# Kernel optimization log

Measured on AMD Instinct MI355X. Metric: run time of the kernel, lower is better.

The kernel has to match this reference:

```python
import jax, jax.numpy as jnp
import numpy as np

B, S, E, H = 2, 2048, 1024, 16
HD = E // H  # head dim = 64
BASE = 10000.0


def _rope(x):
    # x: [b, h, s, hd]; interleaved RoPE (pairs (2i, 2i+1) rotated)
    s, hd = x.shape[-2], x.shape[-1]
    theta = 1.0 / (BASE ** (jnp.arange(0, hd, 2, dtype=jnp.float32) / hd))  # [hd/2]
    enc = jnp.arange(s, dtype=jnp.float32)[:, None] * theta[None, :]        # [s, hd/2]
    enc = jnp.repeat(enc, 2, axis=-1)                                        # [s, hd] interleaved
    cos, sin = jnp.cos(enc), jnp.sin(enc)
    # rotate_half: (x1, x2) -> (-x2, x1) on interleaved pairs
    xp = x.reshape(*x.shape[:-1], hd // 2, 2)
    rot = jnp.stack((-xp[..., 1], xp[..., 0]), axis=-1).reshape(x.shape)
    return x * cos + rot * sin


def reference(x, w1, w2):
    b, s, e = x.shape
    qkv = jnp.einsum('bse,fe->bsf', x, w1)                 # [b, s, 3e]
    qkv = qkv.reshape(b, s, 3, H, HD)                      # 'b s (n h e)'
    q, k, v = (jnp.transpose(qkv[:, :, i], (0, 2, 1, 3)) for i in range(3))  # [b,h,s,hd]
    q, k = _rope(q), _rope(k)
    scale = 1.0 / jnp.sqrt(jnp.asarray(HD, dtype=x.dtype))
    scores = jnp.einsum('bhqd,bhkd->bhqk', q, k) * scale   # [b,h,s,s]
    attn = jax.nn.softmax(scores, axis=-1)
    o = jnp.einsum('bhqk,bhkd->bhqd', attn, v)             # [b,h,s,hd]
    o = jnp.transpose(o, (0, 2, 1, 3)).reshape(b, s, e)    # 'b h s e -> b s (h e)'
    return jnp.einsum('bse,fe->bsf', o, w2)


def setup_inputs() -> dict:
    key = jax.random.key(0)
    k1, k2, k3 = jax.random.split(key, 3)
    x = jax.random.normal(k1, (B, S, E), dtype=jnp.float32)
    w1 = jax.random.normal(k2, (3 * E, E), dtype=jnp.float32) * (E ** -0.5)
    w2 = jax.random.normal(k3, (E, E), dtype=jnp.float32) * (E ** -0.5)
    return {"x": x, "w1": w1, "w2": w2}
```

## Files before the change

kernel.cpp:

```cpp
#include <hip/hip_runtime.h>
#include <math.h>

typedef unsigned short u16;
typedef unsigned int u32;
typedef float f32x4 __attribute__((ext_vector_type(4)));
typedef float f32x16 __attribute__((ext_vector_type(16)));
typedef u32 u32x4 __attribute__((ext_vector_type(4)));

static const size_t TAB_B  = 0;
static const size_t QBF_B  = 524288;
static const size_t KBF_B  = 8912896;
static const size_t VTB_B  = 17301504;
static const size_t W2H_B  = 25690112;
static const size_t XBF_B  = 29884416;
static const size_t W1BF_B = 38273024;
static const size_t O16_B  = 29884416;

#if __has_builtin(__builtin_amdgcn_exp2f)
#define EXP2(x) __builtin_amdgcn_exp2f(x)
#else
#define EXP2(x) __expf(0.69314718056f * (x))
#endif

__device__ __forceinline__ u16 f2bf(float f) {
  u32 u = __builtin_bit_cast(u32, f);
  u += 0x7fffu + ((u >> 16) & 1u);
  return (u16)(u >> 16);
}
__device__ __forceinline__ float bf2f(u16 h) {
  return __builtin_bit_cast(float, (u32)h << 16);
}
__device__ __forceinline__ u16 f2h(float f) {
  _Float16 h = (_Float16)f;
  return __builtin_bit_cast(u16, h);
}
__device__ __forceinline__ u32 cvtpk(float a, float b) {
  u32 r;
  asm("v_cvt_pk_bf16_f32 %0, %1, %2" : "=v"(r) : "v"(a), "v"(b));
  return r;
}
__device__ __forceinline__ void plswap(u32& a, u32& b) {
  asm volatile("v_permlane32_swap_b32 %0, %1" : "+v"(a), "+v"(b));
}
__device__ __forceinline__ void mfma16(f32x4& d, u32x4 a, u32x4 b) {
  asm volatile("v_mfma_f32_16x16x32_bf16 %0, %1, %2, %0"
               : "+v"(d)
               : "v"(a), "v"(b));
}
__device__ __forceinline__ void mfma16f(f32x4& d, u32x4 a, u32x4 b) {
  asm volatile("v_mfma_f32_16x16x32_f16 %0, %1, %2, %0"
               : "+v"(d)
               : "v"(a), "v"(b));
}
__device__ __forceinline__ void mfma32(f32x16& d, u32x4 a, u32x4 b) {
  asm volatile("v_mfma_f32_32x32x16_bf16 %0, %1, %2, %0"
               : "+v"(d)
               : "v"(a), "v"(b));
}
__device__ __forceinline__ void gld16(const void* g, void* l) {
  __builtin_amdgcn_global_load_lds(
      (const __attribute__((address_space(1))) void*)(void*)g,
      (__attribute__((address_space(3))) void*)l, 16, 0, 0);
}
#define HZ()                                            \
  do {                                                  \
    asm volatile("s_nop 7\ns_nop 7\ns_nop 7\ns_nop 7"); \
    __builtin_amdgcn_sched_barrier(0);                  \
  } while (0)

__global__ __launch_bounds__(256) void prep_kernel(
    const float* __restrict__ x, const float* __restrict__ w1,
    const float* __restrict__ w2, float2* __restrict__ tab,
    u16* __restrict__ xbf, u16* __restrict__ w1bf, u16* __restrict__ w2h) {
  const int blk = blockIdx.x;
  const int t = threadIdx.x;
  if (blk < 256) {
    const int idx = (blk << 8) + t;
    const int s = idx >> 5, i = idx & 31;
    double theta = pow(10000.0, -((double)(2 * i)) / 64.0);
    float ang = (float)s * (float)theta;
    tab[idx] = make_float2(cosf(ang), sinf(ang));
  } else if (blk < 1280) {
    int i = ((blk - 256) << 8) + t;
#pragma unroll
    for (int r = 0; r < 4; ++r, i += 262144) {
      float4 v = ((const float4*)x)[i];
      ushort4 o;
      o.x = f2bf(v.x); o.y = f2bf(v.y); o.z = f2bf(v.z); o.w = f2bf(v.w);
      ((ushort4*)xbf)[i] = o;
    }
  } else if (blk < 2048) {
    int i = ((blk - 1280) << 8) + t;
#pragma unroll
    for (int r = 0; r < 4; ++r, i += 196608) {
      float4 v = ((const float4*)w1)[i];
      ushort4 o;
      o.x = f2bf(v.x); o.y = f2bf(v.y); o.z = f2bf(v.z); o.w = f2bf(v.w);
      ((ushort4*)w1bf)[i] = o;
    }
  } else {
    int i = ((blk - 2048) << 8) + t;
#pragma unroll
    for (int r = 0; r < 4; ++r, i += 65536) {
      float4 v = ((const float4*)w2)[i];
      ushort4 o;
      o.x = f2h(v.x); o.y = f2h(v.y); o.z = f2h(v.z); o.w = f2h(v.w);
      ((ushort4*)w2h)[i] = o;
    }
  }
}

template <int MODE>
__global__ __launch_bounds__(256) void gemm_bt(
    const u16* __restrict__ Ahi, const u16* __restrict__ Bhi, int nbn, int nkb,
    int cpx, const float2* __restrict__ tab, u16* __restrict__ qd,
    u16* __restrict__ kd, u16* __restrict__ vtd, float* __restrict__ fout) {
  __shared__ __align__(16) char SMEM[34816];
  char* As = SMEM;
  char* Bs = SMEM + 16384;
  const int bid = blockIdx.x;
  const int wgid = (bid & 7) * cpx + (bid >> 3);
  const int bm = wgid / nbn;
  const int bn = wgid % nbn;
  const int m0 = bm << 7;
  const int n0 = bn << 7;
  const int t = threadIdx.x;
  const int w = t >> 6;
  const int lane = t & 63;
  const int lr = lane & 15;
  const int lg = lane >> 4;
  const int wr0 = (w >> 1) << 6;
  const int wc0 = (w & 1) << 6;
  const int srow0 = t >> 3;
  const int sblk = t & 7;

  f32x4 acc[4][4];
#pragma unroll
  for (int mi = 0; mi < 4; ++mi)
#pragma unroll
    for (int ni = 0; ni < 4; ++ni) acc[mi][ni] = (f32x4)0.0f;

  for (int kb = 0; kb < nkb; ++kb) {
    const int k0 = kb << 6;
    if (kb) __syncthreads();
#pragma unroll
    for (int r = 0; r < 4; ++r) {
      const int row = srow0 + (r << 5);
      const int g = sblk ^ (row & 7);
      gld16(Ahi + (size_t)(m0 + row) * 1024 + k0 + (g << 3),
            As + (r << 12) + (w << 10));
      gld16(Bhi + (size_t)(n0 + row) * 1024 + k0 + (g << 3),
            Bs + (r << 12) + (w << 10));
    }
    asm volatile("s_waitcnt vmcnt(0)" ::: "memory");
    __syncthreads();
#pragma unroll
    for (int kk = 0; kk < 2; ++kk) {
      u32x4 af[4], bf[4];
#pragma unroll
      for (int mi = 0; mi < 4; ++mi) {
        const int row = wr0 + (mi << 4) + lr;
        af[mi] = *(const u32x4*)(As + row * 128 +
                                 ((((kk << 2) + lg) ^ (row & 7)) << 4));
      }
#pragma unroll
      for (int ni = 0; ni < 4; ++ni) {
        const int row = wc0 + (ni << 4) + lr;
        bf[ni] = *(const u32x4*)(Bs + row * 128 +
                                 ((((kk << 2) + lg) ^ (row & 7)) << 4));
      }
      asm volatile("s_nop 1");
      __builtin_amdgcn_s_setprio(1);
#pragma unroll
      for (int mi = 0; mi < 4; ++mi)
#pragma unroll
        for (int ni = 0; ni < 4; ++ni) {
          if constexpr (MODE == 1)
            mfma16f(acc[mi][ni], af[mi], bf[ni]);
          else
            mfma16(acc[mi][ni], af[mi], bf[ni]);
        }
      __builtin_amdgcn_s_setprio(0);
    }
  }
  HZ();
  if (MODE == 0 && n0 >= 2048) {
    u16* Vt = (u16*)SMEM;
    __syncthreads();
#pragma unroll
    for (int mi = 0; mi < 4; ++mi)
#pragma unroll
      for (int ni = 0; ni < 4; ++ni)
#pragma unroll
        for (int i = 0; i < 4; ++i) {
          const int dl = wc0 + (ni << 4) + lr;
          const int sl = wr0 + (mi << 4) + (lg << 2) + i;
          Vt[dl * 136 + sl] = f2bf(acc[mi][ni][i]);
        }
    __syncthreads();
    const int row = t >> 1;
    const int half = t & 1;
    const int hh2 = (n0 - 2048 + row) >> 6;
    const int d2 = (n0 - 2048 + row) & 63;
    const int b2 = m0 >> 11;
    u16* dst = vtd + (((size_t)(b2 * 16 + hh2) * 64 + d2) * 2048) +
               (m0 & 2047) + half * 64;
    const u16* src = Vt + row * 136 + half * 64;
#pragma unroll
    for (int c = 0; c < 8; ++c)
      *(u32x4*)(dst + (c << 3)) = *(const u32x4*)(src + (c << 3));
    return;
  }
#pragma unroll
  for (int mi = 0; mi < 4; ++mi)
#pragma unroll
    for (int ni = 0; ni < 4; ++ni)
#pragma unroll
      for (int i = 0; i < 4; ++i) {
        float val = acc[mi][ni][i];
        const int grow = m0 + wr0 + (mi << 4) + (lg << 2) + i;
        const int col = n0 + wc0 + (ni << 4) + lr;
        if (MODE == 0) {
          const int b = grow >> 11, s = grow & 2047;
          const int which = col >> 10, hh = (col >> 6) & 15, d = col & 63;
          const size_t base = (size_t)((b << 4) + hh);
          float other = __shfl_xor(val, 1);
          float2 cs = tab[(s << 5) + (d >> 1)];
          float r = (d & 1) ? fmaf(val, cs.x, other * cs.y)
                            : fmaf(val, cs.x, -other * cs.y);
          if (which == 0) r *= 0.18033688011f;
          u16* dstp = which ? kd : qd;
          dstp[(base * 2048 + s) * 64 + d] = f2bf(r);
        } else {
          fout[(size_t)grow * 1024 + col] = val;
        }
      }
}

__global__ __launch_bounds__(256) void attn_mfma(
    const u16* __restrict__ q, const u16* __restrict__ k,
    const u16* __restrict__ vt, u16* __restrict__ o16) {
  __shared__ __align__(16) char Ks[2][8192];
  __shared__ __align__(16) char Vs[2][8192];
  const int bid = blockIdx.x;
  const int swz = (bid & 7) * 64 + (bid >> 3);
  const int qt = swz & 15;
  const int hh = (swz >> 4) & 15;
  const int b = swz >> 8;
  const int t = threadIdx.x;
  const int w = t >> 6;
  const int lane = t & 63;
  const int lq = lane & 31;
  const int h = lane >> 5;

  const size_t bh = (size_t)((b << 4) + hh);
  const u16* qb = q + (bh * 2048 + (size_t)(qt * 128 + w * 32)) * 64;
  const u16* kb = k + bh * 2048 * 64;
  const u16* vb = vt + bh * 64 * 2048;

  u32x4 qf[4];
#pragma unroll
  for (int dk = 0; dk < 4; ++dk)
    qf[dk] = *(const u32x4*)(qb + lq * 64 + dk * 16 + h * 8);

  auto issue = [&](int kt_, int buf_) {
    const u16* ksrc = kb + kt_ * 4096;
#pragma unroll
    for (int r = 0; r < 2; ++r) {
      const int row = (t >> 3) + (r << 5);
      const int g = (t & 7) ^ (row & 7);
      gld16(ksrc + row * 64 + (g << 3), &Ks[buf_][(r << 12) + (w << 10)]);
      gld16(vb + (size_t)row * 2048 + kt_ * 64 + (g << 3),
            &Vs[buf_][(r << 12) + (w << 10)]);
    }
  };

  f32x16 oacc0 = (f32x16)0.0f, oacc1 = (f32x16)0.0f;
  float lrow = 0.0f;

  issue(0, 0);
  for (int kt = 0; kt < 32; ++kt) {
    const int cur = kt & 1;
    if (kt < 31) {
      issue(kt + 1, cur ^ 1);
      asm volatile("s_waitcnt vmcnt(4)" ::: "memory");
    } else {
      asm volatile("s_waitcnt vmcnt(0)" ::: "memory");
    }
    __syncthreads();
    const char* Kc = Ks[cur];
    const char* Vc = Vs[cur];
    f32x16 s0 = (f32x16)0.0f, s1 = (f32x16)0.0f;
    __builtin_amdgcn_s_setprio(1);
#pragma unroll
    for (int dk = 0; dk < 4; ++dk) {
      const int c = (dk << 1) + h;
      u32x4 kf0 = *(const u32x4*)(Kc + lq * 128 + ((c ^ (lq & 7)) << 4));
      u32x4 kf1 = *(const u32x4*)(Kc + (32 + lq) * 128 + ((c ^ (lq & 7)) << 4));
      mfma32(s0, kf0, qf[dk]);
      mfma32(s1, kf1, qf[dk]);
    }
    __builtin_amdgcn_s_setprio(0);
    HZ();
    float lsum = 0.0f;
#pragma unroll
    for (int i = 0; i < 16; ++i) {
      s0[i] = EXP2(s0[i]);
      lsum += s0[i];
    }
#pragma unroll
    for (int i = 0; i < 16; ++i) {
      s1[i] = EXP2(s1[i]);
      lsum += s1[i];
    }
    lrow += lsum;
    u32x4 pa0, pa1, pa2, pa3;
    {
      u32 w0 = cvtpk(s0[0], s0[1]), w1 = cvtpk(s0[2], s0[3]);
      u32 w2 = cvtpk(s0[4], s0[5]), w3 = cvtpk(s0[6], s0[7]);
      u32 w4 = cvtpk(s0[8], s0[9]), w5 = cvtpk(s0[10], s0[11]);
      u32 w6 = cvtpk(s0[12], s0[13]), w7 = cvtpk(s0[14], s0[15]);
      plswap(w0, w2);
      plswap(w1, w3);
      plswap(w4, w6);
      plswap(w5, w7);
      pa0[0] = w0; pa0[1] = w1; pa0[2] = w2; pa0[3] = w3;
      pa1[0] = w4; pa1[1] = w5; pa1[2] = w6; pa1[3] = w7;
      u32 y0 = cvtpk(s1[0], s1[1]), y1 = cvtpk(s1[2], s1[3]);
      u32 y2 = cvtpk(s1[4], s1[5]), y3 = cvtpk(s1[6], s1[7]);
      u32 y4 = cvtpk(s1[8], s1[9]), y5 = cvtpk(s1[10], s1[11]);
      u32 y6 = cvtpk(s1[12], s1[13]), y7 = cvtpk(s1[14], s1[15]);
      plswap(y0, y2);
      plswap(y1, y3);
      plswap(y4, y6);
      plswap(y5, y7);
      pa2[0] = y0; pa2[1] = y1; pa2[2] = y2; pa2[3] = y3;
      pa3[0] = y4; pa3[1] = y5; pa3[2] = y6; pa3[3] = y7;
    }
    asm volatile("s_nop 2");
    __builtin_amdgcn_s_setprio(1);
#define PVSTEP(kbk, paf)                                                      \
  {                                                                           \
    const int c = ((kbk) << 1) + h;                                           \
    u32x4 vf0 = *(const u32x4*)(Vc + lq * 128 + ((c ^ (lq & 7)) << 4));       \
    u32x4 vf1 =                                                               \
        *(const u32x4*)(Vc + (32 + lq) * 128 + ((c ^ (lq & 7)) << 4));        \
    mfma32(oacc0, paf, vf0);                                                  \
    mfma32(oacc1, paf, vf1);                                                  \
  }
    PVSTEP(0, pa0)
    PVSTEP(1, pa1)
    PVSTEP(2, pa2)
    PVSTEP(3, pa3)
#undef PVSTEP
    __builtin_amdgcn_s_setprio(0);
    __syncthreads();
  }
  HZ();
  const float invl = 1.0f / (lrow + __shfl_xor(lrow, 32));
#pragma unroll
  for (int r = 0; r < 16; ++r) {
    const int qr = (r & 3) + 8 * (r >> 2) + 4 * h;
    const float fr = __shfl(invl, qr);
    const size_t srow = (size_t)(b * 2048 + (qt << 7) + (w << 5) + qr);
    const size_t base = srow * 1024 + (hh << 6) + lq;
    o16[base] = f2h(oacc0[r] * fr);
    o16[base + 32] = f2h(oacc1[r] * fr);
  }
}

extern "C" void kernel_launch(void* const* d_in, const int* in_sizes, int n_in,
                              void* d_out, int out_size, void* d_ws,
                              size_t ws_size, hipStream_t stream) {
  const float* x = (const float*)d_in[0];
  const float* w1 = (const float*)d_in[1];
  const float* w2 = (const float*)d_in[2];
  char* ws = (char*)d_ws;
  float2* tab = (float2*)(ws + TAB_B);
  u16* qbf = (u16*)(ws + QBF_B);
  u16* kbf = (u16*)(ws + KBF_B);
  u16* vtbf = (u16*)(ws + VTB_B);
  u16* w2h = (u16*)(ws + W2H_B);
  u16* xbf = (u16*)(ws + XBF_B);
  u16* w1bf = (u16*)(ws + W1BF_B);
  u16* o16 = (u16*)(ws + O16_B);
  float* out = (float*)d_out;

  prep_kernel<<<dim3(2304), dim3(256), 0, stream>>>(x, w1, w2, tab, xbf, w1bf,
                                                    w2h);
  gemm_bt<0><<<dim3(32 * 24), dim3(256), 0, stream>>>(
      xbf, w1bf, 24, 16, 96, tab, qbf, kbf, vtbf, nullptr);
  attn_mfma<<<dim3(512), dim3(256), 0, stream>>>(qbf, kbf, vtbf, o16);
  gemm_bt<1><<<dim3(32 * 8), dim3(256), 0, stream>>>(
      o16, w2h, 8, 16, 32, nullptr, nullptr, nullptr, nullptr, out);
}
```

Measured before the change: 111.1 us.

## Narrow output-projection GEMM tiles and compute softmax row sums via MFMA

Templates the GEMM on the N-tile width and launches the output projection with 128x64 tiles, doubling the number of workgroups (512 instead of 256) so more compute units stay busy. In the attention kernel, the per-thread scalar accumulation of exp values is replaced by an extra MFMA against a ones vector, so row sums come out in the same layout as the output accumulator and the final cross-lane shuffles go away. The row sums are now built from the bf16-rounded probabilities, which matches the values used in P·V. The trade-off is extra MFMA work per step and smaller GEMM tiles with less operand reuse.

```diff
diff --git a/kernel.cpp b/kernel.cpp
--- a/kernel.cpp
+++ b/kernel.cpp
@@ -110,12 +110,12 @@
   }
 }
 
-template <int MODE>
+template <int MODE, int NI>
 __global__ __launch_bounds__(256) void gemm_bt(
     const u16* __restrict__ Ahi, const u16* __restrict__ Bhi, int nbn, int nkb,
     int cpx, const float2* __restrict__ tab, u16* __restrict__ qd,
     u16* __restrict__ kd, u16* __restrict__ vtd, float* __restrict__ fout) {
-  __shared__ __align__(16) char SMEM[34816];
+  __shared__ __align__(16) char SMEM[MODE == 0 ? 34816 : 16384 + NI * 4096];
   char* As = SMEM;
   char* Bs = SMEM + 16384;
   const int bid = blockIdx.x;
@@ -123,22 +123,22 @@
   const int bm = wgid / nbn;
   const int bn = wgid % nbn;
   const int m0 = bm << 7;
-  const int n0 = bn << 7;
+  const int n0 = bn * (NI << 5);
   const int t = threadIdx.x;
   const int w = t >> 6;
   const int lane = t & 63;
   const int lr = lane & 15;
   const int lg = lane >> 4;
   const int wr0 = (w >> 1) << 6;
-  const int wc0 = (w & 1) << 6;
+  const int wc0 = (w & 1) * (NI << 4);
   const int srow0 = t >> 3;
   const int sblk = t & 7;
 
-  f32x4 acc[4][4];
+  f32x4 acc[4][NI];
 #pragma unroll
   for (int mi = 0; mi < 4; ++mi)
 #pragma unroll
-    for (int ni = 0; ni < 4; ++ni) acc[mi][ni] = (f32x4)0.0f;
+    for (int ni = 0; ni < NI; ++ni) acc[mi][ni] = (f32x4)0.0f;
 
   for (int kb = 0; kb < nkb; ++kb) {
     const int k0 = kb << 6;
@@ -149,6 +149,11 @@
       const int g = sblk ^ (row & 7);
       gld16(Ahi + (size_t)(m0 + row) * 1024 + k0 + (g << 3),
             As + (r << 12) + (w << 10));
+    }
+#pragma unroll
+    for (int r = 0; r < NI; ++r) {
+      const int row = srow0 + (r << 5);
+      const int g = sblk ^ (row & 7);
       gld16(Bhi + (size_t)(n0 + row) * 1024 + k0 + (g << 3),
             Bs + (r << 12) + (w << 10));
     }
@@ -156,7 +161,7 @@
     __syncthreads();
 #pragma unroll
     for (int kk = 0; kk < 2; ++kk) {
-      u32x4 af[4], bf[4];
+      u32x4 af[4], bf[NI];
 #pragma unroll
       for (int mi = 0; mi < 4; ++mi) {
         const int row = wr0 + (mi << 4) + lr;
@@ -164,7 +169,7 @@
                                  ((((kk << 2) + lg) ^ (row & 7)) << 4));
       }
 #pragma unroll
-      for (int ni = 0; ni < 4; ++ni) {
+      for (int ni = 0; ni < NI; ++ni) {
         const int row = wc0 + (ni << 4) + lr;
         bf[ni] = *(const u32x4*)(Bs + row * 128 +
                                  ((((kk << 2) + lg) ^ (row & 7)) << 4));
@@ -174,7 +179,7 @@
 #pragma unroll
       for (int mi = 0; mi < 4; ++mi)
 #pragma unroll
-        for (int ni = 0; ni < 4; ++ni) {
+        for (int ni = 0; ni < NI; ++ni) {
           if constexpr (MODE == 1)
             mfma16f(acc[mi][ni], af[mi], bf[ni]);
           else
@@ -184,37 +189,39 @@
     }
   }
   HZ();
-  if (MODE == 0 && n0 >= 2048) {
-    u16* Vt = (u16*)SMEM;
-    __syncthreads();
-#pragma unroll
-    for (int mi = 0; mi < 4; ++mi)
-#pragma unroll
-      for (int ni = 0; ni < 4; ++ni)
-#pragma unroll
-        for (int i = 0; i < 4; ++i) {
-          const int dl = wc0 + (ni << 4) + lr;
-          const int sl = wr0 + (mi << 4) + (lg << 2) + i;
-          Vt[dl * 136 + sl] = f2bf(acc[mi][ni][i]);
-        }
-    __syncthreads();
-    const int row = t >> 1;
-    const int half = t & 1;
-    const int hh2 = (n0 - 2048 + row) >> 6;
-    const int d2 = (n0 - 2048 + row) & 63;
-    const int b2 = m0 >> 11;
-    u16* dst = vtd + (((size_t)(b2 * 16 + hh2) * 64 + d2) * 2048) +
-               (m0 & 2047) + half * 64;
-    const u16* src = Vt + row * 136 + half * 64;
-#pragma unroll
-    for (int c = 0; c < 8; ++c)
-      *(u32x4*)(dst + (c << 3)) = *(const u32x4*)(src + (c << 3));
-    return;
+  if constexpr (MODE == 0) {
+    if (n0 >= 2048) {
+      u16* Vt = (u16*)SMEM;
+      __syncthreads();
+#pragma unroll
+      for (int mi = 0; mi < 4; ++mi)
+#pragma unroll
+        for (int ni = 0; ni < NI; ++ni)
+#pragma unroll
+          for (int i = 0; i < 4; ++i) {
+            const int dl = wc0 + (ni << 4) + lr;
+            const int sl = wr0 + (mi << 4) + (lg << 2) + i;
+            Vt[dl * 136 + sl] = f2bf(acc[mi][ni][i]);
+          }
+      __syncthreads();
+      const int row = t >> 1;
+      const int half = t & 1;
+      const int hh2 = (n0 - 2048 + row) >> 6;
+      const int d2 = (n0 - 2048 + row) & 63;
+      const int b2 = m0 >> 11;
+      u16* dst = vtd + (((size_t)(b2 * 16 + hh2) * 64 + d2) * 2048) +
+                 (m0 & 2047) + half * 64;
+      const u16* src = Vt + row * 136 + half * 64;
+#pragma unroll
+      for (int c = 0; c < 8; ++c)
+        *(u32x4*)(dst + (c << 3)) = *(const u32x4*)(src + (c << 3));
+      return;
+    }
   }
 #pragma unroll
   for (int mi = 0; mi < 4; ++mi)
 #pragma unroll
-    for (int ni = 0; ni < 4; ++ni)
+    for (int ni = 0; ni < NI; ++ni)
 #pragma unroll
       for (int i = 0; i < 4; ++i) {
         float val = acc[mi][ni][i];
@@ -276,7 +283,8 @@
   };
 
   f32x16 oacc0 = (f32x16)0.0f, oacc1 = (f32x16)0.0f;
-  float lrow = 0.0f;
+  f32x16 lacc = (f32x16)0.0f;
+  const u32x4 ones = {0x3F803F80u, 0x3F803F80u, 0x3F803F80u, 0x3F803F80u};
 
   issue(0, 0);
   for (int kt = 0; kt < 32; ++kt) {
@@ -302,18 +310,10 @@
     }
     __builtin_amdgcn_s_setprio(0);
     HZ();
-    float lsum = 0.0f;
-#pragma unroll
-    for (int i = 0; i < 16; ++i) {
-      s0[i] = EXP2(s0[i]);
-      lsum += s0[i];
-    }
-#pragma unroll
-    for (int i = 0; i < 16; ++i) {
-      s1[i] = EXP2(s1[i]);
-      lsum += s1[i];
-    }
-    lrow += lsum;
+#pragma unroll
+    for (int i = 0; i < 16; ++i) s0[i] = EXP2(s0[i]);
+#pragma unroll
+    for (int i = 0; i < 16; ++i) s1[i] = EXP2(s1[i]);
     u32x4 pa0, pa1, pa2, pa3;
     {
       u32 w0 = cvtpk(s0[0], s0[1]), w1 = cvtpk(s0[2], s0[3]);
@@ -347,6 +347,7 @@
         *(const u32x4*)(Vc + (32 + lq) * 128 + ((c ^ (lq & 7)) << 4));        \
     mfma32(oacc0, paf, vf0);                                                  \
     mfma32(oacc1, paf, vf1);                                                  \
+    mfma32(lacc, paf, ones);                                                  \
   }
     PVSTEP(0, pa0)
     PVSTEP(1, pa1)
@@ -357,11 +358,10 @@
     __syncthreads();
   }
   HZ();
-  const float invl = 1.0f / (lrow + __shfl_xor(lrow, 32));
 #pragma unroll
   for (int r = 0; r < 16; ++r) {
     const int qr = (r & 3) + 8 * (r >> 2) + 4 * h;
-    const float fr = __shfl(invl, qr);
+    const float fr = 1.0f / lacc[r];
     const size_t srow = (size_t)(b * 2048 + (qt << 7) + (w << 5) + qr);
     const size_t base = srow * 1024 + (hh << 6) + lq;
     o16[base] = f2h(oacc0[r] * fr);
@@ -388,9 +388,9 @@
 
   prep_kernel<<<dim3(2304), dim3(256), 0, stream>>>(x, w1, w2, tab, xbf, w1bf,
                                                     w2h);
-  gemm_bt<0><<<dim3(32 * 24), dim3(256), 0, stream>>>(
+  gemm_bt<0, 4><<<dim3(32 * 24), dim3(256), 0, stream>>>(
       xbf, w1bf, 24, 16, 96, tab, qbf, kbf, vtbf, nullptr);
   attn_mfma<<<dim3(512), dim3(256), 0, stream>>>(qbf, kbf, vtbf, o16);
-  gemm_bt<1><<<dim3(32 * 8), dim3(256), 0, stream>>>(
-      o16, w2h, 8, 16, 32, nullptr, nullptr, nullptr, nullptr, out);
-}
+  gemm_bt<1, 2><<<dim3(32 * 16), dim3(256), 0, stream>>>(
+      o16, w2h, 16, 16, 64, nullptr, nullptr, nullptr, nullptr, out);
+}
```

After: 109.0 us. Within noise of the previous version (-1.9%).
